# Kernel optimization log

Hardware: AMD Instinct MI355X
Metric: run time of the kernel (lower is better)

## Reference

```python
import jax, jax.numpy as jnp
import numpy as np

NUM_HEADS = 8
HEAD_DIM = 16  # hidden_size 128 / 8 heads
SCALE = float(np.sqrt(HEAD_DIM))


def setup_inputs() -> dict:
    key = jax.random.key(0)
    k1, k2, k3, k4 = jax.random.split(key, 4)
    B, N, H = 1, 50000, 128
    E = 800000
    q = jax.random.normal(k1, (B, N, H), dtype=jnp.float32)
    k = jax.random.normal(k2, (B, N, H), dtype=jnp.float32)
    v = jax.random.normal(k3, (B, N, H), dtype=jnp.float32)
    edge_index = jax.random.randint(k4, (2, E), 0, N, dtype=jnp.int64)
    return {"q": q, "k": k, "v": v, "edge_index": edge_index}


def reference(q, k, v, edge_index):
    B, N, H = q.shape
    total = B * N
    qh = q.reshape(total, NUM_HEADS, HEAD_DIM)
    kh = k.reshape(total, NUM_HEADS, HEAD_DIM)
    vh = v.reshape(total, NUM_HEADS, HEAD_DIM)
    src_idx = edge_index[0]
    dst_idx = edge_index[1]
    src = kh[src_idx]          # [E, heads, d]
    dest = qh[dst_idx]         # [E, heads, d]
    # per-edge scaled dot score, clamped then exponentiated
    score = jnp.sum(src * dest / SCALE, axis=-1, keepdims=True)  # [E, heads, 1]
    score = jnp.exp(jnp.clip(score, -5.0, 5.0))
    msg = vh[src_idx] * score  # [E, heads, d]
    wV = jax.ops.segment_sum(msg, dst_idx, num_segments=total)    # [total, heads, d]
    Z = jax.ops.segment_sum(score, dst_idx, num_segments=total)   # [total, heads, 1]
    x = wV / (Z + 1e-6)
    return x.reshape(B, N, NUM_HEADS * HEAD_DIM)
```

## Files before the change

kernel.cpp:

```cpp
#include <hip/hip_runtime.h>

#define HID 128
#define CHUNK 16384
#define CSHIFT 14
#define MAXW 25088

typedef unsigned short u16;
typedef unsigned int u32;

__device__ __forceinline__ float bf2f(u16 u) { return __uint_as_float(((u32)u) << 16); }
__device__ __forceinline__ float lof(u32 w) { return __uint_as_float(w << 16); }
__device__ __forceinline__ float hif(u32 w) { return __uint_as_float(w & 0xFFFF0000u); }
__device__ __forceinline__ u16 f2bf(float f) {
    u32 x = __float_as_uint(f);
    return (u16)((x + 0x7FFF + ((x >> 16) & 1)) >> 16);
}

__global__ void pack_kernel(const float* __restrict__ k, const float* __restrict__ v,
                            u16* __restrict__ kv, int N) {
    int g = blockIdx.x * 256 + threadIdx.x;
    int node = g >> 6, l = g & 63;
    if (node >= N) return;
    float2 kk = ((const float2*)(k + (long long)node * HID))[l];
    float2 vv = ((const float2*)(v + (long long)node * HID))[l];
    ushort4 o;
    o.x = f2bf(kk.x * 0.25f);
    o.y = f2bf(kk.y * 0.25f);
    o.z = f2bf(vv.x);
    o.w = f2bf(vv.y);
    ((ushort4*)(kv + (long long)node * 256))[l] = o;
}

__global__ __launch_bounds__(1024) void hist_kernel(const int* __restrict__ ei,
        u32* __restrict__ Hp, u16* __restrict__ lrank, int E, int W) {
    __shared__ u32 hcnt[MAXW];
    int c = blockIdx.x;
    for (int j = threadIdx.x; j < W; j += 1024) hcnt[j] = 0;
    __syncthreads();
    int beg = c << CSHIFT;
    int end = min(E, beg + CHUNK);
    for (int i = beg + (int)threadIdx.x; i < end; i += 1024) {
        int d = ei[E + i];
        u32 sh = (u32)(d & 1) << 4;
        u32 old = atomicAdd(&hcnt[d >> 1], 1u << sh);
        lrank[i] = (u16)((old >> sh) & 0xFFFFu);
    }
    __syncthreads();
    for (int j = threadIdx.x; j < W; j += 1024) Hp[(size_t)c * W + j] = hcnt[j];
}

__global__ void scan_node_kernel(u32* __restrict__ Hp, u32* __restrict__ t,
                                 int W, int NB, int N) {
    int j = blockIdx.x * blockDim.x + threadIdx.x;
    if (j >= W) return;
    u32 lo = 0, hi = 0;
    for (int c = 0; c < NB; c++) {
        size_t idx = (size_t)c * W + j;
        u32 w = Hp[idx];
        Hp[idx] = lo | (hi << 16);
        lo += w & 0xFFFFu;
        hi += w >> 16;
    }
    int n0 = 2 * j, n1 = 2 * j + 1;
    if (n0 < N) t[n0] = lo;
    if (n1 < N) t[n1] = hi;
}

__global__ void scanA_kernel(const u32* __restrict__ counts, int* __restrict__ offsets,
                             int* __restrict__ partials, int M) {
    __shared__ int sdata[256];
    int tid = threadIdx.x;
    int base = blockIdx.x * 2048 + tid * 8;
    int v[8];
    int tsum = 0;
    for (int j = 0; j < 8; j++) {
        int idx = base + j;
        v[j] = (idx < M) ? (int)counts[idx] : 0;
        tsum += v[j];
    }
    sdata[tid] = tsum;
    __syncthreads();
    for (int off = 1; off < 256; off <<= 1) {
        int x = sdata[tid];
        int y = (tid >= off) ? sdata[tid - off] : 0;
        __syncthreads();
        sdata[tid] = x + y;
        __syncthreads();
    }
    int excl = sdata[tid] - tsum;
    for (int j = 0; j < 8; j++) {
        int idx = base + j;
        if (idx < M) offsets[idx] = excl;
        excl += v[j];
    }
    if (tid == 255) partials[blockIdx.x] = sdata[255];
}

__global__ void scanC_kernel(int* __restrict__ offsets, const int* __restrict__ partials,
                             int M, int E, int nbA) {
    __shared__ int sp[256];
    int tid = threadIdx.x;
    if (tid == 0) {
        int run = 0;
        for (int i = 0; i < nbA; i++) { sp[i] = run; run += partials[i]; }
    }
    __syncthreads();
    int idx = blockIdx.x * blockDim.x + tid;
    if (idx < M) offsets[idx] += sp[idx >> 11];
    if (idx == 0) offsets[M] = E;
}

__global__ void scatter_kernel(const int* __restrict__ ei, const u32* __restrict__ Hp,
                               const u16* __restrict__ lrank, const int* __restrict__ offsets,
                               u16* __restrict__ srcs, int E, int W) {
    int e = blockIdx.x * blockDim.x + threadIdx.x;
    if (e >= E) return;
    int c = e >> CSHIFT;
    int d = ei[E + e];
    u32 sh = (u32)(d & 1) << 4;
    u32 b = (Hp[(size_t)c * W + (d >> 1)] >> sh) & 0xFFFFu;
    int pos = offsets[d] + (int)b + (int)lrank[e];
    srcs[pos] = (u16)ei[e];
}

__global__ __launch_bounds__(128) void reduce_packed(
        const float* __restrict__ q, const u16* __restrict__ kv,
        const int* __restrict__ offsets, const u16* __restrict__ srcs,
        float* __restrict__ out, int N) {
    int node = blockIdx.x * 2 + (threadIdx.x >> 6);
    if (node >= N) return;
    int l = threadIdx.x & 63;
    int m = l & 31;
    int half = l >> 5;

    float4 qv = ((const float4*)(q + (long long)node * HID))[m];
    const char* kvb = (const char*)kv;
    u32 laneoff = (u32)m << 4;
    float4 acc = make_float4(0.0f, 0.0f, 0.0f, 0.0f);
    float z = 0.0f;

    int beg = offsets[node];
    int end = offsets[node + 1];
    int i = beg;

#define GLOAD(s_) (*(const uint4*)(kvb + (((u32)(s_) << 9) + laneoff)))

    for (; i + 8 <= end; i += 8) {
        u32 sA0 = srcs[i + 0], sB0 = srcs[i + 1];
        u32 sA1 = srcs[i + 2], sB1 = srcs[i + 3];
        u32 sA2 = srcs[i + 4], sB2 = srcs[i + 5];
        u32 sA3 = srcs[i + 6], sB3 = srcs[i + 7];
        uint4 a0 = GLOAD(half ? sB0 : sA0);
        uint4 a1 = GLOAD(half ? sB1 : sA1);
        uint4 a2 = GLOAD(half ? sB2 : sA2);
        uint4 a3 = GLOAD(half ? sB3 : sA3);

        float p0 = lof(a0.x) * qv.x + hif(a0.x) * qv.y + lof(a0.z) * qv.z + hif(a0.z) * qv.w;
        float p1 = lof(a1.x) * qv.x + hif(a1.x) * qv.y + lof(a1.z) * qv.z + hif(a1.z) * qv.w;
        float p2 = lof(a2.x) * qv.x + hif(a2.x) * qv.y + lof(a2.z) * qv.z + hif(a2.z) * qv.w;
        float p3 = lof(a3.x) * qv.x + hif(a3.x) * qv.y + lof(a3.z) * qv.z + hif(a3.z) * qv.w;

        p0 += __shfl_xor(p0, 1); p1 += __shfl_xor(p1, 1);
        p2 += __shfl_xor(p2, 1); p3 += __shfl_xor(p3, 1);
        p0 += __shfl_xor(p0, 2); p1 += __shfl_xor(p1, 2);
        p2 += __shfl_xor(p2, 2); p3 += __shfl_xor(p3, 2);

        float c0 = __expf(fminf(fmaxf(p0, -5.0f), 5.0f));
        float c1 = __expf(fminf(fmaxf(p1, -5.0f), 5.0f));
        float c2 = __expf(fminf(fmaxf(p2, -5.0f), 5.0f));
        float c3 = __expf(fminf(fmaxf(p3, -5.0f), 5.0f));

        acc.x += lof(a0.y) * c0 + lof(a1.y) * c1 + lof(a2.y) * c2 + lof(a3.y) * c3;
        acc.y += hif(a0.y) * c0 + hif(a1.y) * c1 + hif(a2.y) * c2 + hif(a3.y) * c3;
        acc.z += lof(a0.w) * c0 + lof(a1.w) * c1 + lof(a2.w) * c2 + lof(a3.w) * c3;
        acc.w += hif(a0.w) * c0 + hif(a1.w) * c1 + hif(a2.w) * c2 + hif(a3.w) * c3;
        z += c0 + c1 + c2 + c3;
    }
    for (; i < end; i += 2) {
        int idx = i + half;
        bool ok = idx < end;
        u32 s = srcs[ok ? idx : i];
        uint4 a = GLOAD(s);
        float p = lof(a.x) * qv.x + hif(a.x) * qv.y + lof(a.z) * qv.z + hif(a.z) * qv.w;
        p += __shfl_xor(p, 1);
        p += __shfl_xor(p, 2);
        float c = __expf(fminf(fmaxf(p, -5.0f), 5.0f));
        c = ok ? c : 0.0f;
        acc.x += lof(a.y) * c;
        acc.y += hif(a.y) * c;
        acc.z += lof(a.w) * c;
        acc.w += hif(a.w) * c;
        z += c;
    }
#undef GLOAD

    acc.x += __shfl_xor(acc.x, 32);
    acc.y += __shfl_xor(acc.y, 32);
    acc.z += __shfl_xor(acc.z, 32);
    acc.w += __shfl_xor(acc.w, 32);
    z     += __shfl_xor(z, 32);

    if (half == 0) {
        float inv = 1.0f / (z + 1e-6f);
        ((float4*)(out + (long long)node * HID))[m] =
            make_float4(acc.x * inv, acc.y * inv, acc.z * inv, acc.w * inv);
    }
}


__global__ void count_kernel(const int* __restrict__ ei, int* __restrict__ counts,
                             int* __restrict__ pos, int E) {
    int e = blockIdx.x * blockDim.x + threadIdx.x;
    if (e < E) pos[e] = atomicAdd(&counts[ei[E + e]], 1);
}

__global__ void fill_kernel(const int* __restrict__ ei, const int* __restrict__ offsets,
                            const int* __restrict__ pos, int* __restrict__ srcs, int E) {
    int e = blockIdx.x * blockDim.x + threadIdx.x;
    if (e < E) srcs[offsets[ei[E + e]] + pos[e]] = ei[e];
}

__global__ __launch_bounds__(256) void reduce_f32(
        const float* __restrict__ q, const float* __restrict__ k,
        const float* __restrict__ v, const int* __restrict__ offsets,
        const int* __restrict__ srcs, float* __restrict__ out, int N) {
    int node = blockIdx.x * 4 + (threadIdx.x >> 6);
    if (node >= N) return;
    int l = threadIdx.x & 63;
    float2 qv = ((const float2*)(q + (long long)node * HID))[l];
    float accx = 0.0f, accy = 0.0f, z = 0.0f;
    int beg = offsets[node], end = offsets[node + 1];
    for (int i = beg; i < end; i++) {
        int s = srcs[i];
        float2 kk = ((const float2*)(k + (long long)s * HID))[l];
        float2 vv = ((const float2*)(v + (long long)s * HID))[l];
        float p = (kk.x * qv.x + kk.y * qv.y) * 0.25f;
        p += __shfl_xor(p, 1);
        p += __shfl_xor(p, 2);
        p += __shfl_xor(p, 4);
        float c = __expf(fminf(fmaxf(p, -5.0f), 5.0f));
        accx += vv.x * c; accy += vv.y * c; z += c;
    }
    float inv = 1.0f / (z + 1e-6f);
    ((float2*)(out + (long long)node * HID))[l] = make_float2(accx * inv, accy * inv);
}

extern "C" void kernel_launch(void* const* d_in, const int* in_sizes, int n_in,
                              void* d_out, int out_size, void* d_ws, size_t ws_size,
                              hipStream_t stream) {
    const float* q = (const float*)d_in[0];
    const float* k = (const float*)d_in[1];
    const float* v = (const float*)d_in[2];
    const int* ei = (const int*)d_in[3];
    float* out = (float*)d_out;

    int E = in_sizes[3] / 2;
    int N = in_sizes[0] / HID;

    int block = 256;
    int eblocks = (E + block - 1) / block;
    int nbA = (N + 2047) / 2048;
    int nblocksN = (N + 255) / 256;

    int W = (N + 1) / 2;
    int NB = (E + CHUNK - 1) >> CSHIFT;

    size_t kv_bytes = (size_t)N * 256 * sizeof(u16);
    size_t need = kv_bytes + ((size_t)NB * W + N + N + 1 + 256) * 4
                + 2 * ((size_t)E + 8) * 2 + 64;

    bool primary = (W <= MAXW) && (nbA <= 256) && (ws_size >= need);

    if (primary) {
        u16* kv = (u16*)d_ws;
        u32* Hp = (u32*)((char*)d_ws + kv_bytes);
        u32* t = Hp + (size_t)NB * W;
        int* offsets = (int*)(t + N);
        int* partials = offsets + N + 1;
        u16* lrank = (u16*)(partials + 256);
        u16* srcs = lrank + ((E + 8) & ~1);

        pack_kernel<<<(N * 64 + 255) / 256, 256, 0, stream>>>(k, v, kv, N);
        hist_kernel<<<NB, 1024, 0, stream>>>(ei, Hp, lrank, E, W);
        scan_node_kernel<<<(W + 255) / 256, 256, 0, stream>>>(Hp, t, W, NB, N);
        scanA_kernel<<<nbA, 256, 0, stream>>>(t, offsets, partials, N);
        scanC_kernel<<<nblocksN, 256, 0, stream>>>(offsets, partials, N, E, nbA);
        scatter_kernel<<<eblocks, 256, 0, stream>>>(ei, Hp, lrank, offsets, srcs, E, W);
        int rgrid = (N + 1) / 2;
        reduce_packed<<<rgrid, 128, 0, stream>>>(q, kv, offsets, srcs, out, N);
    } else {
        int* counts = (int*)d_ws;
        int* offsets = counts + N;
        int* partials = offsets + N + 1;
        int* pos = partials + 256;
        int* srcs = pos + E;

        hipMemsetAsync(counts, 0, (size_t)N * sizeof(int), stream);
        count_kernel<<<eblocks, 256, 0, stream>>>(ei, counts, pos, E);
        scanA_kernel<<<nbA, 256, 0, stream>>>((const u32*)counts, offsets, partials, N);
        scanC_kernel<<<nblocksN, 256, 0, stream>>>(offsets, partials, N, E, nbA);
        fill_kernel<<<eblocks, 256, 0, stream>>>(ei, offsets, pos, srcs, E);
        int rgrid = (N + 3) / 4;
        reduce_f32<<<rgrid, 256, 0, stream>>>(q, k, v, offsets, srcs, out, N);
    }
}
```

Measured before the change: 122.3 us.

## Merge scan into single block and fuse pack with scatter kernel

Replaces the two-kernel scan (scanA + scanC) with a single 1024-thread block scan, and folds the K/V bf16 packing into the scatter kernel as extra blocks in one grid. This cuts the primary path's launch count from seven kernels to five and lets the packing work overlap with the scatter. The single-block scan serialises about 49 elements per thread, which may be slower than the parallel two-pass scan. The new primary condition is always true, so the fallback path is chosen only by the width and workspace checks.

```diff
diff --git a/kernel.cpp b/kernel.cpp
--- a/kernel.cpp
+++ b/kernel.cpp
@@ -14,21 +14,6 @@
 __device__ __forceinline__ u16 f2bf(float f) {
     u32 x = __float_as_uint(f);
     return (u16)((x + 0x7FFF + ((x >> 16) & 1)) >> 16);
-}
-
-__global__ void pack_kernel(const float* __restrict__ k, const float* __restrict__ v,
-                            u16* __restrict__ kv, int N) {
-    int g = blockIdx.x * 256 + threadIdx.x;
-    int node = g >> 6, l = g & 63;
-    if (node >= N) return;
-    float2 kk = ((const float2*)(k + (long long)node * HID))[l];
-    float2 vv = ((const float2*)(v + (long long)node * HID))[l];
-    ushort4 o;
-    o.x = f2bf(kk.x * 0.25f);
-    o.y = f2bf(kk.y * 0.25f);
-    o.z = f2bf(vv.x);
-    o.w = f2bf(vv.y);
-    ((ushort4*)(kv + (long long)node * 256))[l] = o;
 }
 
 __global__ __launch_bounds__(1024) void hist_kernel(const int* __restrict__ ei,
@@ -66,61 +51,59 @@
     if (n1 < N) t[n1] = hi;
 }
 
-__global__ void scanA_kernel(const u32* __restrict__ counts, int* __restrict__ offsets,
-                             int* __restrict__ partials, int M) {
-    __shared__ int sdata[256];
+__global__ __launch_bounds__(1024) void scanOne_kernel(const u32* __restrict__ t,
+        int* __restrict__ offsets, int N, int E) {
+    __shared__ int sdata[1024];
     int tid = threadIdx.x;
-    int base = blockIdx.x * 2048 + tid * 8;
-    int v[8];
-    int tsum = 0;
-    for (int j = 0; j < 8; j++) {
-        int idx = base + j;
-        v[j] = (idx < M) ? (int)counts[idx] : 0;
-        tsum += v[j];
-    }
-    sdata[tid] = tsum;
-    __syncthreads();
-    for (int off = 1; off < 256; off <<= 1) {
+    int per = (N + 1023) / 1024;
+    int beg = tid * per;
+    int end = min(N, beg + per);
+    int s = 0;
+    for (int i = beg; i < end; i++) s += (int)t[i];
+    sdata[tid] = s;
+    __syncthreads();
+    for (int off = 1; off < 1024; off <<= 1) {
         int x = sdata[tid];
         int y = (tid >= off) ? sdata[tid - off] : 0;
         __syncthreads();
         sdata[tid] = x + y;
         __syncthreads();
     }
-    int excl = sdata[tid] - tsum;
-    for (int j = 0; j < 8; j++) {
-        int idx = base + j;
-        if (idx < M) offsets[idx] = excl;
-        excl += v[j];
-    }
-    if (tid == 255) partials[blockIdx.x] = sdata[255];
-}
-
-__global__ void scanC_kernel(int* __restrict__ offsets, const int* __restrict__ partials,
-                             int M, int E, int nbA) {
-    __shared__ int sp[256];
-    int tid = threadIdx.x;
-    if (tid == 0) {
-        int run = 0;
-        for (int i = 0; i < nbA; i++) { sp[i] = run; run += partials[i]; }
-    }
-    __syncthreads();
-    int idx = blockIdx.x * blockDim.x + tid;
-    if (idx < M) offsets[idx] += sp[idx >> 11];
-    if (idx == 0) offsets[M] = E;
-}
-
-__global__ void scatter_kernel(const int* __restrict__ ei, const u32* __restrict__ Hp,
-                               const u16* __restrict__ lrank, const int* __restrict__ offsets,
-                               u16* __restrict__ srcs, int E, int W) {
-    int e = blockIdx.x * blockDim.x + threadIdx.x;
-    if (e >= E) return;
-    int c = e >> CSHIFT;
-    int d = ei[E + e];
-    u32 sh = (u32)(d & 1) << 4;
-    u32 b = (Hp[(size_t)c * W + (d >> 1)] >> sh) & 0xFFFFu;
-    int pos = offsets[d] + (int)b + (int)lrank[e];
-    srcs[pos] = (u16)ei[e];
+    int excl = sdata[tid] - s;
+    for (int i = beg; i < end; i++) {
+        offsets[i] = excl;
+        excl += (int)t[i];
+    }
+    if (tid == 1023) offsets[N] = E;
+}
+
+__global__ void packscatter_kernel(const float* __restrict__ k, const float* __restrict__ v,
+                                   u16* __restrict__ kv, const int* __restrict__ ei,
+                                   const u32* __restrict__ Hp, const u16* __restrict__ lrank,
+                                   const int* __restrict__ offsets, u16* __restrict__ srcs,
+                                   int N, int E, int W, int packBlocks) {
+    if ((int)blockIdx.x < packBlocks) {
+        int g = blockIdx.x * 256 + threadIdx.x;
+        int node = g >> 6, l = g & 63;
+        if (node >= N) return;
+        float2 kk = ((const float2*)(k + (long long)node * HID))[l];
+        float2 vv = ((const float2*)(v + (long long)node * HID))[l];
+        ushort4 o;
+        o.x = f2bf(kk.x * 0.25f);
+        o.y = f2bf(kk.y * 0.25f);
+        o.z = f2bf(vv.x);
+        o.w = f2bf(vv.y);
+        ((ushort4*)(kv + (long long)node * 256))[l] = o;
+    } else {
+        int e = (blockIdx.x - packBlocks) * 256 + threadIdx.x;
+        if (e >= E) return;
+        int c = e >> CSHIFT;
+        int d = ei[E + e];
+        u32 sh = (u32)(d & 1) << 4;
+        u32 b = (Hp[(size_t)c * W + (d >> 1)] >> sh) & 0xFFFFu;
+        int pos = offsets[d] + (int)b + (int)lrank[e];
+        srcs[pos] = (u16)ei[e];
+    }
 }
 
 __global__ __launch_bounds__(128) void reduce_packed(
@@ -245,6 +228,50 @@
     ((float2*)(out + (long long)node * HID))[l] = make_float2(accx * inv, accy * inv);
 }
 
+__global__ void scanA_kernel(const u32* __restrict__ counts, int* __restrict__ offsets,
+                             int* __restrict__ partials, int M) {
+    __shared__ int sdata[256];
+    int tid = threadIdx.x;
+    int base = blockIdx.x * 2048 + tid * 8;
+    int v[8];
+    int tsum = 0;
+    for (int j = 0; j < 8; j++) {
+        int idx = base + j;
+        v[j] = (idx < M) ? (int)counts[idx] : 0;
+        tsum += v[j];
+    }
+    sdata[tid] = tsum;
+    __syncthreads();
+    for (int off = 1; off < 256; off <<= 1) {
+        int x = sdata[tid];
+        int y = (tid >= off) ? sdata[tid - off] : 0;
+        __syncthreads();
+        sdata[tid] = x + y;
+        __syncthreads();
+    }
+    int excl = sdata[tid] - tsum;
+    for (int j = 0; j < 8; j++) {
+        int idx = base + j;
+        if (idx < M) offsets[idx] = excl;
+        excl += v[j];
+    }
+    if (tid == 255) partials[blockIdx.x] = sdata[255];
+}
+
+__global__ void scanC_kernel(int* __restrict__ offsets, const int* __restrict__ partials,
+                             int M, int E, int nbA) {
+    __shared__ int sp[256];
+    int tid = threadIdx.x;
+    if (tid == 0) {
+        int run = 0;
+        for (int i = 0; i < nbA; i++) { sp[i] = run; run += partials[i]; }
+    }
+    __syncthreads();
+    int idx = blockIdx.x * blockDim.x + tid;
+    if (idx < M) offsets[idx] += sp[idx >> 11];
+    if (idx == 0) offsets[M] = E;
+}
+
 extern "C" void kernel_launch(void* const* d_in, const int* in_sizes, int n_in,
                               void* d_out, int out_size, void* d_ws, size_t ws_size,
                               hipStream_t stream) {
@@ -257,8 +284,7 @@
     int E = in_sizes[3] / 2;
     int N = in_sizes[0] / HID;
 
-    int block = 256;
-    int eblocks = (E + block - 1) / block;
+    int eblocks = (E + 255) / 256;
     int nbA = (N + 2047) / 2048;
     int nblocksN = (N + 255) / 256;
 
@@ -269,7 +295,7 @@
     size_t need = kv_bytes + ((size_t)NB * W + N + N + 1 + 256) * 4
                 + 2 * ((size_t)E + 8) * 2 + 64;
 
-    bool primary = (W <= MAXW) && (nbA <= 256) && (ws_size >= need);
+    bool primary = (W <= MAXW) && (N <= 1024 * ((N + 1023) / 1024)) && (ws_size >= need);
 
     if (primary) {
         u16* kv = (u16*)d_ws;
@@ -280,12 +306,13 @@
         u16* lrank = (u16*)(partials + 256);
         u16* srcs = lrank + ((E + 8) & ~1);
 
-        pack_kernel<<<(N * 64 + 255) / 256, 256, 0, stream>>>(k, v, kv, N);
+        int packBlocks = (N * 64 + 255) / 256;
+
         hist_kernel<<<NB, 1024, 0, stream>>>(ei, Hp, lrank, E, W);
         scan_node_kernel<<<(W + 255) / 256, 256, 0, stream>>>(Hp, t, W, NB, N);
-        scanA_kernel<<<nbA, 256, 0, stream>>>(t, offsets, partials, N);
-        scanC_kernel<<<nblocksN, 256, 0, stream>>>(offsets, partials, N, E, nbA);
-        scatter_kernel<<<eblocks, 256, 0, stream>>>(ei, Hp, lrank, offsets, srcs, E, W);
+        scanOne_kernel<<<1, 1024, 0, stream>>>(t, offsets, N, E);
+        packscatter_kernel<<<packBlocks + eblocks, 256, 0, stream>>>(
+            k, v, kv, ei, Hp, lrank, offsets, srcs, N, E, W, packBlocks);
         int rgrid = (N + 1) / 2;
         reduce_packed<<<rgrid, 128, 0, stream>>>(q, kv, offsets, srcs, out, N);
     } else {
```

Result: slower. 187.2 us (+53.1%).
